# Performance work log

Hardware: AMD Instinct MI355X
Metric: run time of the kernel (lower is better)

The kernel has to match this reference:

```python
import jax, jax.numpy as jnp
import numpy as np

B, F, H, E = 16, 128, 144, 24   # batch, frames, num_harmonies, embedding
C0, C1 = 12, 12                 # harmony component dims (root, quality)


def setup_inputs() -> dict:
    key = jax.random.key(0)
    ks = jax.random.split(key, 7)
    note_embedding_seq = jax.random.normal(ks[0], (B, F, E), jnp.float32)
    # one-hot harmony vectors: concat(one_hot(root), one_hot(quality))
    idx = np.arange(H)
    hv = np.zeros((H, E), np.float32)
    hv[idx, idx // C1] = 1.0
    hv[idx, C0 + idx % C1] = 1.0
    harmony_vector = jnp.asarray(np.broadcast_to(hv, (B, H, E)).copy())
    s = 1.0 / np.sqrt(E)
    W0 = jax.random.uniform(ks[1], (C0, C0), jnp.float32, -s, s)
    b0 = jax.random.uniform(ks[2], (C0,), jnp.float32, -s, s)
    W1 = jax.random.uniform(ks[3], (C1, C1), jnp.float32, -s, s)
    b1 = jax.random.uniform(ks[4], (C1,), jnp.float32, -s, s)
    Wc = jax.random.uniform(ks[5], (E, E), jnp.float32, -s, s)
    bc = jax.random.uniform(ks[6], (E,), jnp.float32, -s, s)
    return {"note_embedding_seq": note_embedding_seq, "harmony_vector": harmony_vector,
            "W0": W0, "b0": b0, "W1": W1, "b1": b1, "Wc": Wc, "bc": bc}


def reference(note_embedding_seq, harmony_vector, W0, b0, W1, b1, Wc, bc):
    # HarmonyEncoder: per-component linear then combined linear
    h0 = harmony_vector[..., :C0] @ W0.T + b0
    h1 = harmony_vector[..., C0:] @ W1.T + b1
    q = jnp.concatenate([h0, h1], axis=-1) @ Wc.T + bc          # [B,H,E]

    # Per-segment attention. keys == values, so both the attention logits and
    # the value dot-products reduce to d[b,h,l] = q . k_l.  For segment [s,e]:
    #   score = sum_{l=s..e} softmax_seg(scale*d_l) * d_l
    # which is computed exactly for all segments via cumulative sums.
    scale = 1.0 / jnp.sqrt(jnp.float32(E))
    d = jnp.einsum('bhe,ble->bhl', q, note_embedding_seq)        # [B,H,F]
    m = jnp.max(d * scale, axis=-1, keepdims=True)               # global max: cancels in ratio
    p = jnp.exp(d * scale - m)                                   # [B,H,F]
    num = jnp.cumsum(p * d, axis=-1)                             # [B,H,F]
    den = jnp.cumsum(p, axis=-1)
    num0 = jnp.pad(num, ((0, 0), (0, 0), (1, 0)))[..., :F]       # cumsum up to s-1
    den0 = jnp.pad(den, ((0, 0), (0, 0), (1, 0)))[..., :F]
    dn = num[:, :, None, :] - num0[:, :, :, None]                # [B,H,s,e]
    dd = den[:, :, None, :] - den0[:, :, :, None]
    valid = jnp.triu(jnp.ones((F, F), bool))                     # e >= s
    score = jnp.where(valid, dn / jnp.where(valid, dd, 1.0), 0.0)
    return jnp.transpose(score, (0, 2, 3, 1))                    # [B,F,F,H]
```

## Files before the change

### kernel.cpp

```cpp
#include <hip/hip_runtime.h>
#include <hip/hip_bf16.h>

#define BB 16
#define FF 128
#define HH 144
#define EE 24
#define C0C 12

typedef float v4f __attribute__((ext_vector_type(4)));

#define TABLE_ELEMS (BB * (FF + 1) * HH)

__device__ __forceinline__ float fastdiv(float n, float d) {
    float r = __builtin_amdgcn_rcpf(d);
    r = fmaf(fmaf(-d, r, 1.0f), r, r);
    return n * r;
}

__global__ __launch_bounds__(128) void seg_k1(
    const float* __restrict__ note,
    const float* __restrict__ hv,
    const float* __restrict__ W0,
    const float* __restrict__ b0,
    const float* __restrict__ W1,
    const float* __restrict__ b1,
    const float* __restrict__ Wc,
    const float* __restrict__ bc,
    float* __restrict__ num_t,
    float* __restrict__ den_t)
{
    const int blk = blockIdx.x;
    const int b = blk / HH;
    const int h = blk - b * HH;
    const int tid = threadIdx.x;
    const int lane = tid & 63;

    __shared__ float s_hcat[EE];
    __shared__ float s_q[EE];
    __shared__ float s_wmax[2];
    __shared__ float s_tot[2];

    const float* hvb = hv + ((size_t)b * HH + h) * EE;
    if (tid < C0C) {
        float acc = b0[tid];
        #pragma unroll
        for (int j = 0; j < C0C; ++j) acc += W0[tid * C0C + j] * hvb[j];
        s_hcat[tid] = acc;
    } else if (tid < 2 * C0C) {
        const int i = tid - C0C;
        float acc = b1[i];
        #pragma unroll
        for (int j = 0; j < C0C; ++j) acc += W1[i * C0C + j] * hvb[C0C + j];
        s_hcat[tid] = acc;
    }
    __syncthreads();
    if (tid < EE) {
        float acc = bc[tid];
        #pragma unroll
        for (int j = 0; j < EE; ++j) acc += Wc[tid * EE + j] * s_hcat[j];
        s_q[tid] = acc;
    }
    __syncthreads();

    const float* nr = note + ((size_t)b * FF + tid) * EE;
    float d = 0.f;
    #pragma unroll
    for (int e = 0; e < EE; e += 4) {
        const v4f v = *reinterpret_cast<const v4f*>(nr + e);
        d += s_q[e] * v.x + s_q[e + 1] * v.y + s_q[e + 2] * v.z + s_q[e + 3] * v.w;
    }

    const float scale = 0.20412414523193150818f;
    const float ds = d * scale;

    float m = ds;
    #pragma unroll
    for (int off = 32; off > 0; off >>= 1) m = fmaxf(m, __shfl_xor(m, off));
    if (lane == 0) s_wmax[tid >> 6] = m;
    __syncthreads();
    m = fmaxf(s_wmax[0], s_wmax[1]);

    float p = __expf(ds - m);
    float pd = p * d;

    #pragma unroll
    for (int off = 1; off < 64; off <<= 1) {
        const float a = __shfl_up(p, off);
        const float c = __shfl_up(pd, off);
        if (lane >= off) { p += a; pd += c; }
    }
    if (tid == 63) { s_tot[0] = p; s_tot[1] = pd; }
    __syncthreads();
    if (tid >= 64) { p += s_tot[0]; pd += s_tot[1]; }

    const size_t base = (size_t)b * (FF + 1) * HH + h;
    num_t[base + (size_t)(tid + 1) * HH] = pd;
    den_t[base + (size_t)(tid + 1) * HH] = p;
    if (tid == 0) {
        num_t[base] = 0.f;
        den_t[base] = 0.f;
    }
}

__device__ __forceinline__ void k2_row_half(
    const float* __restrict__ nb, const float* __restrict__ db,
    float* __restrict__ out_b, int s, int tid, int half)
{
    float* ob = out_b + (size_t)s * (FF * HH);

    const int nzr = (s - half + 1) >> 1;
    for (int c = tid; c < nzr * 36; c += 256) {
        const int row2 = c / 36;
        const int col = c - row2 * 36;
        const int row = 2 * row2 + half;
        *reinterpret_cast<v4f*>(ob + (size_t)row * HH + col * 4) = (v4f)(0.f);
    }

    if (tid < 252) {
        const int r = tid / 36;
        const int hq = tid - r * 36;
        const int h = hq * 4;

        const v4f n0 = *reinterpret_cast<const v4f*>(nb + (size_t)s * HH + h);
        const v4f d0 = *reinterpret_cast<const v4f*>(db + (size_t)s * HH + h);

        const int e0 = s + r + 7 * half;
        const float* pn = nb + (size_t)(e0 + 1) * HH + h;
        const float* pd_ = db + (size_t)(e0 + 1) * HH + h;
        float* po = ob + (size_t)e0 * HH + h;

        #pragma unroll 2
        for (int e = e0; e < FF; e += 14) {
            const v4f n1 = *reinterpret_cast<const v4f*>(pn);
            const v4f d1 = *reinterpret_cast<const v4f*>(pd_);
            v4f val;
            val.x = fastdiv(n1.x - n0.x, d1.x - d0.x);
            val.y = fastdiv(n1.y - n0.y, d1.y - d0.y);
            val.z = fastdiv(n1.z - n0.z, d1.z - d0.z);
            val.w = fastdiv(n1.w - n0.w, d1.w - d0.w);
            *reinterpret_cast<v4f*>(po) = val;
            pn += 14 * HH;
            pd_ += 14 * HH;
            po += 14 * HH;
        }
    }
}

__global__ __launch_bounds__(256) void seg_k2(
    const float* __restrict__ num_t,
    const float* __restrict__ den_t,
    float* __restrict__ out)
{
    const int blk = blockIdx.x;
    const int b = blk >> 7;
    const int rest = blk & 127;
    const int sp = rest >> 1;
    const int half = rest & 1;
    const int tid = threadIdx.x;

    const float* nb = num_t + (size_t)b * (FF + 1) * HH;
    const float* db = den_t + (size_t)b * (FF + 1) * HH;
    float* out_b = out + (size_t)b * (FF * FF * HH);

    k2_row_half(nb, db, out_b, sp, tid, half);
    k2_row_half(nb, db, out_b, 127 - sp, tid, half);
}

extern "C" void kernel_launch(void* const* d_in, const int* in_sizes, int n_in,
                              void* d_out, int out_size, void* d_ws, size_t ws_size,
                              hipStream_t stream) {
    const float* note = (const float*)d_in[0];
    const float* hv   = (const float*)d_in[1];
    const float* W0   = (const float*)d_in[2];
    const float* b0   = (const float*)d_in[3];
    const float* W1   = (const float*)d_in[4];
    const float* b1   = (const float*)d_in[5];
    const float* Wc   = (const float*)d_in[6];
    const float* bc   = (const float*)d_in[7];
    float* out = (float*)d_out;

    float* num_t = (float*)d_ws;
    float* den_t = num_t + TABLE_ELEMS;

    seg_k1<<<BB * HH, 128, 0, stream>>>(note, hv, W0, b0, W1, b1, Wc, bc, num_t, den_t);
    seg_k2<<<BB * FF, 256, 0, stream>>>(num_t, den_t, out);
}
```

Measured before the change: 38.32 us.

## Tile k1 over 16 harmonies per block with shared-memory scan and XCD-aware block mapping

The first kernel now handles 16 harmonies of one batch per 256-thread block, down from one harmony per block. Each block stages that batch's note embeddings in shared memory, computes the dot products there, and runs a Hillis-Steele prefix scan in LDS with vectorised table writes. Block indices in both kernels are remapped so that blocks for the same batch land on the same XCD (blk&7), aiming for better L2 locality between k1's table writes and k2's reads. The trade-off is fewer blocks (144) and a scan that needs 14 barriers, against far fewer redundant note loads and q computations.

Result: faster. 36.58 us (-4.5%).

```diff
diff --git a/kernel.cpp b/kernel.cpp
--- a/kernel.cpp
+++ b/kernel.cpp
@@ -17,7 +17,7 @@
     return n * r;
 }
 
-__global__ __launch_bounds__(128) void seg_k1(
+__global__ __launch_bounds__(256) void seg_k1(
     const float* __restrict__ note,
     const float* __restrict__ hv,
     const float* __restrict__ W0,
@@ -30,75 +30,115 @@
     float* __restrict__ den_t)
 {
     const int blk = blockIdx.x;
-    const int b = blk / HH;
-    const int h = blk - b * HH;
+    const int x = blk & 7;
+    const int t = blk >> 3;
+    const int b = 2 * x + (t >= 9);
+    const int tile = (t >= 9) ? t - 9 : t;
+    const int h0 = tile * 16;
     const int tid = threadIdx.x;
-    const int lane = tid & 63;
-
-    __shared__ float s_hcat[EE];
-    __shared__ float s_q[EE];
-    __shared__ float s_wmax[2];
-    __shared__ float s_tot[2];
-
-    const float* hvb = hv + ((size_t)b * HH + h) * EE;
-    if (tid < C0C) {
-        float acc = b0[tid];
-        #pragma unroll
-        for (int j = 0; j < C0C; ++j) acc += W0[tid * C0C + j] * hvb[j];
-        s_hcat[tid] = acc;
-    } else if (tid < 2 * C0C) {
-        const int i = tid - C0C;
-        float acc = b1[i];
-        #pragma unroll
-        for (int j = 0; j < C0C; ++j) acc += W1[i * C0C + j] * hvb[C0C + j];
-        s_hcat[tid] = acc;
-    }
-    __syncthreads();
-    if (tid < EE) {
-        float acc = bc[tid];
-        #pragma unroll
-        for (int j = 0; j < EE; ++j) acc += Wc[tid * EE + j] * s_hcat[j];
-        s_q[tid] = acc;
-    }
-    __syncthreads();
-
-    const float* nr = note + ((size_t)b * FF + tid) * EE;
-    float d = 0.f;
+
+    __shared__ float s_note[FF * EE];
+    __shared__ float s_hcat[16][EE];
+    __shared__ float s_q[16][EE];
+    __shared__ float s_p[FF][16];
+    __shared__ float s_pd[FF][16];
+    __shared__ float s_pm[16][16];
+    __shared__ float s_m[16];
+
+    const float* nb_ = note + (size_t)b * FF * EE;
+    for (int k = tid; k < FF * EE / 4; k += 256)
+        reinterpret_cast<v4f*>(s_note)[k] = reinterpret_cast<const v4f*>(nb_)[k];
+
+    for (int idx = tid; idx < 16 * EE; idx += 256) {
+        const int hl = idx / EE, e = idx - hl * EE;
+        const float* hvb = hv + ((size_t)b * HH + h0 + hl) * EE;
+        float acc;
+        if (e < C0C) {
+            acc = b0[e];
+            #pragma unroll
+            for (int j = 0; j < C0C; ++j) acc += W0[e * C0C + j] * hvb[j];
+        } else {
+            const int e1 = e - C0C;
+            acc = b1[e1];
+            #pragma unroll
+            for (int j = 0; j < C0C; ++j) acc += W1[e1 * C0C + j] * hvb[C0C + j];
+        }
+        s_hcat[hl][e] = acc;
+    }
+    __syncthreads();
+    for (int idx = tid; idx < 16 * EE; idx += 256) {
+        const int hl = idx / EE, e = idx - hl * EE;
+        float acc = bc[e];
+        #pragma unroll
+        for (int j = 0; j < EE; ++j) acc += Wc[e * EE + j] * s_hcat[hl][j];
+        s_q[hl][e] = acc;
+    }
+    __syncthreads();
+
+    const int hl = tid & 15;
+    const int f0 = tid >> 4;
+    const float scale = 0.20412414523193150818f;
+
+    float dv[8];
+    float pmax = -3.4e38f;
     #pragma unroll
-    for (int e = 0; e < EE; e += 4) {
-        const v4f v = *reinterpret_cast<const v4f*>(nr + e);
-        d += s_q[e] * v.x + s_q[e + 1] * v.y + s_q[e + 2] * v.z + s_q[e + 3] * v.w;
-    }
-
-    const float scale = 0.20412414523193150818f;
-    const float ds = d * scale;
-
-    float m = ds;
+    for (int k = 0; k < 8; ++k) {
+        const int f = f0 + (k << 4);
+        float acc = 0.f;
+        #pragma unroll
+        for (int e = 0; e < EE; ++e) acc += s_q[hl][e] * s_note[f * EE + e];
+        dv[k] = acc;
+        pmax = fmaxf(pmax, acc);
+    }
+    s_pm[f0][hl] = pmax * scale;
+    __syncthreads();
+    if (tid < 16) {
+        float m = s_pm[0][tid];
+        #pragma unroll
+        for (int r = 1; r < 16; ++r) m = fmaxf(m, s_pm[r][tid]);
+        s_m[tid] = m;
+    }
+    __syncthreads();
+    const float m = s_m[hl];
+
     #pragma unroll
-    for (int off = 32; off > 0; off >>= 1) m = fmaxf(m, __shfl_xor(m, off));
-    if (lane == 0) s_wmax[tid >> 6] = m;
-    __syncthreads();
-    m = fmaxf(s_wmax[0], s_wmax[1]);
-
-    float p = __expf(ds - m);
-    float pd = p * d;
-
-    #pragma unroll
-    for (int off = 1; off < 64; off <<= 1) {
-        const float a = __shfl_up(p, off);
-        const float c = __shfl_up(pd, off);
-        if (lane >= off) { p += a; pd += c; }
-    }
-    if (tid == 63) { s_tot[0] = p; s_tot[1] = pd; }
-    __syncthreads();
-    if (tid >= 64) { p += s_tot[0]; pd += s_tot[1]; }
-
-    const size_t base = (size_t)b * (FF + 1) * HH + h;
-    num_t[base + (size_t)(tid + 1) * HH] = pd;
-    den_t[base + (size_t)(tid + 1) * HH] = p;
-    if (tid == 0) {
-        num_t[base] = 0.f;
-        den_t[base] = 0.f;
+    for (int k = 0; k < 8; ++k) {
+        const int f = f0 + (k << 4);
+        const float p = __expf(dv[k] * scale - m);
+        s_p[f][hl] = p;
+        s_pd[f][hl] = p * dv[k];
+    }
+    __syncthreads();
+
+    for (int off = 1; off < FF; off <<= 1) {
+        float tp[8], tpd[8];
+        #pragma unroll
+        for (int k = 0; k < 8; ++k) {
+            const int f = f0 + (k << 4);
+            tp[k] = (f >= off) ? s_p[f - off][hl] : 0.f;
+            tpd[k] = (f >= off) ? s_pd[f - off][hl] : 0.f;
+        }
+        __syncthreads();
+        #pragma unroll
+        for (int k = 0; k < 8; ++k) {
+            const int f = f0 + (k << 4);
+            if (f >= off) { s_p[f][hl] += tp[k]; s_pd[f][hl] += tpd[k]; }
+        }
+        __syncthreads();
+    }
+
+    const size_t base = (size_t)b * (FF + 1) * HH + h0;
+    for (int idx4 = tid; idx4 < 512; idx4 += 256) {
+        const int f = idx4 >> 2;
+        const int hh = (idx4 & 3) * 4;
+        *reinterpret_cast<v4f*>(num_t + base + (size_t)(f + 1) * HH + hh) =
+            *reinterpret_cast<const v4f*>(&s_pd[f][hh]);
+        *reinterpret_cast<v4f*>(den_t + base + (size_t)(f + 1) * HH + hh) =
+            *reinterpret_cast<const v4f*>(&s_p[f][hh]);
+    }
+    if (tid < 16) {
+        num_t[base + tid] = 0.f;
+        den_t[base + tid] = 0.f;
     }
 }
 
@@ -152,10 +192,12 @@
     float* __restrict__ out)
 {
     const int blk = blockIdx.x;
-    const int b = blk >> 7;
-    const int rest = blk & 127;
-    const int sp = rest >> 1;
-    const int half = rest & 1;
+    const int x = blk & 7;
+    const int t = blk >> 3;
+    const int b = 2 * x + (t >= 128);
+    const int j = t & 127;
+    const int sp = j >> 1;
+    const int half = j & 1;
     const int tid = threadIdx.x;
 
     const float* nb = num_t + (size_t)b * (FF + 1) * HH;
@@ -182,6 +224,6 @@
     float* num_t = (float*)d_ws;
     float* den_t = num_t + TABLE_ELEMS;
 
-    seg_k1<<<BB * HH, 128, 0, stream>>>(note, hv, W0, b0, W1, b1, Wc, bc, num_t, den_t);
+    seg_k1<<<144, 256, 0, stream>>>(note, hv, W0, b0, W1, b1, Wc, bc, num_t, den_t);
     seg_k2<<<BB * FF, 256, 0, stream>>>(num_t, den_t, out);
 }
```
